# Optimization experiments

Hardware: AMD Instinct MI355X
Metric: run time of the kernel (lower is better)

The kernel has to match this reference:

```python
import jax, jax.numpy as jnp
import numpy as np

D, N = 512, 256          # transition steps, batch
H, L, V = 128, 64, 32000 # h_dim, label_dim, lexicon_size


def _valid_transitions(seed=0):
    # generate a valid shift/reduce schedule: reduce only when stack depth >= 2
    rng = np.random.default_rng(seed)
    ptr = np.zeros(N, np.int64)
    trans = np.zeros((D, N), np.int32)
    for t in range(D):
        r = ((rng.random(N) < 0.6) & (ptr >= 2)).astype(np.int32)
        trans[t] = r
        ptr += 1 - 2 * r  # every step pushes 1; reduce pops 2 first
    return jnp.asarray(trans)


def setup_inputs() -> dict:
    key = jax.random.key(0)
    k1, k2, k3 = jax.random.split(key, 3)
    transitions = _valid_transitions()
    labels_idx = jax.random.randint(k1, (D, N), 0, V, dtype=jnp.int32)
    emb = jax.random.normal(k2, (V, L), jnp.float32) * 0.02
    emb = emb.at[0].set(0.0)  # padding_idx=0
    arg_dim = L + 2 * H
    W = jax.random.normal(k3, (arg_dim, 5 * H), jnp.float32) / np.sqrt(arg_dim).astype(np.float32)
    b = jnp.zeros((5 * H,), jnp.float32)
    leaf = jnp.zeros((H,), jnp.float32)  # leaf_input placeholder vector
    return {"transitions": transitions, "labels_idx": labels_idx,
            "emb": emb, "W": W, "b": b, "leaf": leaf}


def _cell(x, hl, hr, cl, cr, W, b):
    # binary TreeLSTM (Tai et al.): gates from concat(label, h_left, h_right)
    g = jnp.concatenate([x, hl, hr], axis=-1) @ W + b  # [N, 5H]
    i, fl, fr, o, u = jnp.split(g, 5, axis=-1)
    c = jax.nn.sigmoid(i) * jnp.tanh(u) + jax.nn.sigmoid(fl) * cl + jax.nn.sigmoid(fr) * cr
    h = jax.nn.sigmoid(o) * jnp.tanh(c)
    return c, h


def reference(transitions, labels_idx, emb, W, b, leaf):
    labels = emb[labels_idx]  # [D,N,L]
    bidx = jnp.arange(N)

    def step(carry, inp):
        h_st, c_st, idx_st, ptr = carry  # [D,N,H],[D,N,H],[D,N],[N]
        t, mask, lab = inp
        mf = mask.astype(bool)[:, None]
        # right popped first, then left (matches _get_indices call order)
        ridx = idx_st[(ptr - 1) % D, bidx]
        lidx = idx_st[(ptr - 2) % D, bidx]
        hl = jnp.where(mf, h_st[lidx, bidx], leaf)
        hr = jnp.where(mf, h_st[ridx, bidx], leaf)
        cl = jnp.where(mf, c_st[lidx, bidx], leaf)
        cr = jnp.where(mf, c_st[ridx, bidx], leaf)
        c, h = _cell(lab, hl, hr, cl, cr, W, b)
        h_st = h_st.at[t].set(h)   # embeddings_stack[step] = h
        c_st = c_st.at[t].set(c)   # cells_stack[step] = c
        newptr = ptr - 2 * mask    # pops (if reduce)
        idx_st = idx_st.at[newptr, bidx].set(t)  # push current step for all batch
        return (h_st, c_st, idx_st, newptr + 1), None

    h_st = jnp.zeros((D, N, H), jnp.float32)
    c_st = jnp.zeros((D, N, H), jnp.float32)
    idx_st = jnp.zeros((D, N), jnp.int32)
    ptr = jnp.zeros((N,), jnp.int32)
    (h_st, c_st, _, _), _ = jax.lax.scan(
        step, (h_st, c_st, idx_st, ptr),
        (jnp.arange(D, dtype=jnp.int32), transitions, labels))
    # original returns (thin_stack[1][D-1], thin_stack[0][D-1]) = (cells, embeddings)
    return c_st[D - 1], h_st[D - 1]
```

## Files before the change

### kernel.cpp

```cpp
#include <hip/hip_runtime.h>
#include <stdint.h>


#define D     512
#define HD    128
#define LD    64
#define NTHR  512
#define GPR   328

typedef unsigned long long u64t;

__device__ __forceinline__ float sigf(float x){ return 1.0f/(1.0f+__expf(-x)); }
__device__ __forceinline__ float tanh_(float x){ return 1.0f-2.0f/(__expf(2.0f*x)+1.0f); }
__device__ __forceinline__ u64t gld64(const float* p){
  return __hip_atomic_load((const u64t*)p, __ATOMIC_RELAXED, __HIP_MEMORY_SCOPE_AGENT);
}
__device__ __forceinline__ u64t gld64u(const unsigned* p){
  return __hip_atomic_load((const u64t*)p, __ATOMIC_RELAXED, __HIP_MEMORY_SCOPE_AGENT);
}
__device__ __forceinline__ void gst32(float* p, float v){
  __hip_atomic_store(p, v, __ATOMIC_RELAXED, __HIP_MEMORY_SCOPE_AGENT);
}
__device__ __forceinline__ void gsttag(unsigned* p, unsigned v){
  __hip_atomic_store(p, v, __ATOMIC_RELAXED, __HIP_MEMORY_SCOPE_AGENT);
}

__global__ __launch_bounds__(NTHR,2) void spinn_kernel(
    const int* __restrict__ trans, const int* __restrict__ labels,
    const float* __restrict__ emb, const float* __restrict__ W,
    const float* __restrict__ bias, const float* __restrict__ leaf,
    float* __restrict__ out, unsigned* __restrict__ tags,
    float* __restrict__ rec, float* __restrict__ cown)
{
  const int bid = blockIdx.x;
  const int g2 = bid>>1, sl = bid&1, ps = sl^1;
  const int gb0 = g2*2;
  const int tid = threadIdx.x;
  const int kg = tid>>6, lane = tid&63;
  const int cq = lane;

  __shared__ __align__(16) float xs[2][2][320];
  __shared__ __align__(16) float gpq[16][GPR];
  __shared__ float bsl[320];
  __shared__ float lshd[HD];
  __shared__ float clb[2][2][64];
  __shared__ uint8_t mS[D][2];
  __shared__ short liA[D][2];
  __shared__ unsigned short stk_[2][D];

  float4 wr4[40]; float wr1[40];
  {
    const int gq = (cq>>4)*128 + sl*64 + ((cq*4)&63);
    const int gu = 512 + sl*64 + cq;
#pragma unroll
    for (int j=0;j<40;++j){
      int k = kg*40 + j;
      wr4[j] = *(const float4*)(W + (size_t)k*640 + gq);
      wr1[j] = W[(size_t)k*640 + gu];
    }
  }
  if (tid < 320){
    int c = tid;
    int gc = (c < 256) ? ((c>>6)*128 + sl*64 + (c&63)) : (512 + sl*64 + (c-256));
    bsl[c] = bias[gc];
  }
  if (tid < HD) lshd[tid] = leaf[tid];
  if (tid < 2){
    int b = tid, p = 0;
    for (int t=0;t<D;++t){
      int m = trans[t*256 + gb0 + b];
      short li = 0;
      if (m) li = (short)stk_[b][p-2];
      mS[t][b] = (uint8_t)m; liA[t][b] = li;
      int np = p - 2*m; stk_[b][np] = (unsigned short)t; p = np+1;
    }
  }
  __syncthreads();

  for (int idx = tid; idx < 640; idx += NTHR){
    int b = (idx >= 320) ? 1 : 0;
    int r = idx - b*320;
    if (r < 64){
      int row = labels[gb0 + b];
      xs[0][b][r] = emb[(size_t)row*LD + r];
    } else {
      xs[0][b][r] = lshd[(r-64)&127];
    }
  }
  __syncthreads();

  auto gemm = [&](int cur){
    float4 a0 = {0.f,0.f,0.f,0.f}, a1 = {0.f,0.f,0.f,0.f};
    float u0 = 0.f, u1 = 0.f;
#pragma unroll
    for (int j4=0;j4<10;++j4){
      int k = kg*40 + j4*4;
      float4 x0 = *(const float4*)&xs[cur][0][k];
      float4 x1 = *(const float4*)&xs[cur][1][k];
      float xa0[4] = {x0.x,x0.y,x0.z,x0.w};
      float xa1[4] = {x1.x,x1.y,x1.z,x1.w};
#pragma unroll
      for (int jj=0;jj<4;++jj){
        float4 w = wr4[j4*4+jj];
        float wu = wr1[j4*4+jj];
        a0.x = __builtin_fmaf(w.x, xa0[jj], a0.x);
        a0.y = __builtin_fmaf(w.y, xa0[jj], a0.y);
        a0.z = __builtin_fmaf(w.z, xa0[jj], a0.z);
        a0.w = __builtin_fmaf(w.w, xa0[jj], a0.w);
        a1.x = __builtin_fmaf(w.x, xa1[jj], a1.x);
        a1.y = __builtin_fmaf(w.y, xa1[jj], a1.y);
        a1.z = __builtin_fmaf(w.z, xa1[jj], a1.z);
        a1.w = __builtin_fmaf(w.w, xa1[jj], a1.w);
        u0 = __builtin_fmaf(wu, xa0[jj], u0);
        u1 = __builtin_fmaf(wu, xa1[jj], u1);
      }
    }
    *(float4*)&gpq[kg*2+0][cq*4] = a0;
    *(float4*)&gpq[kg*2+1][cq*4] = a1;
    gpq[kg*2+0][256+cq] = u0;
    gpq[kg*2+1][256+cq] = u1;
  };

  float ccprev = 0.f;

  for (int t=0;t<D;++t){
    const int cur = t&1, nxt = cur^1;

    if (kg < 4){
      gemm(cur);
    } else if (kg == 4){
      if (t+1 < D){
        int b = lane>>5, jj = lane&31;
        int row = labels[(t+1)*256 + gb0 + b];
        float2 ev = *(const float2*)(emb + (size_t)row*LD + jj*2);
        xs[nxt][b][jj*2]   = ev.x;
        xs[nxt][b][jj*2+1] = ev.y;
      }
    } else if (kg == 5){
      if (t+1 < D){
        int b = lane>>5, jj = lane&31;
        int m1 = mS[t+1][b]; int li = liA[t+1][b];
        if (m1){
          if (li <= t-2){
            size_t ro = (((size_t)li*128+g2)*2 + sl)*128 + b*64 + jj*2;
            union{u64t u; float f[2];} h_, c_;
            h_.u = gld64(rec + ro);
            c_.u = gld64(cown + ro);
            xs[nxt][b][64+sl*64+jj*2]   = h_.f[0];
            xs[nxt][b][64+sl*64+jj*2+1] = h_.f[1];
            clb[nxt][b][jj*2]   = c_.f[0];
            clb[nxt][b][jj*2+1] = c_.f[1];
          }
        } else {
          xs[nxt][b][64+sl*64+jj*2]   = lshd[sl*64+jj*2];
          xs[nxt][b][64+sl*64+jj*2+1] = lshd[sl*64+jj*2+1];
          clb[nxt][b][jj*2]   = lshd[sl*64+jj*2];
          clb[nxt][b][jj*2+1] = lshd[sl*64+jj*2+1];
        }
      }
    } else if (kg == 6){
      if (t+1 < D){
        int b = lane>>5, jj = lane&31;
        int m1 = mS[t+1][b]; int li = liA[t+1][b];
        if (m1){
          if (li <= t-2){
            size_t ro = (((size_t)li*128+g2)*2 + ps)*128 + b*64 + jj*2;
            union{u64t u; float f[2];} h_;
            h_.u = gld64(rec + ro);
            xs[nxt][b][64+ps*64+jj*2]   = h_.f[0];
            xs[nxt][b][64+ps*64+jj*2+1] = h_.f[1];
          }
        } else {
          xs[nxt][b][64+ps*64+jj*2]    = lshd[ps*64+jj*2];
          xs[nxt][b][64+ps*64+jj*2+1]  = lshd[ps*64+jj*2+1];
          xs[nxt][b][192+ps*64+jj*2]   = lshd[ps*64+jj*2];
          xs[nxt][b][192+ps*64+jj*2+1] = lshd[ps*64+jj*2+1];
        }
      }
    } else {
      if (t > 0){
        const unsigned* tp = tags + (((size_t)(t-1)*128+g2)*2 + ps)*16;
        u64t want = ((u64t)(unsigned)(t-1) << 32) | (unsigned)(t-1);
        int it = 0;
        while (gld64u(tp) != want){
          __builtin_amdgcn_s_sleep(1);
          if (++it > (1<<20)) break;
        }
        int b = lane>>5, jj = lane&31;
        size_t ro = (((size_t)(t-1)*128+g2)*2 + ps)*128 + lane*2;
        union{u64t u; float f[2];} h_;
        h_.u = gld64(rec + ro);
        if (mS[t][b]){
          xs[cur][b][192+ps*64+jj*2]   = h_.f[0];
          xs[cur][b][192+ps*64+jj*2+1] = h_.f[1];
        }
        if (t+1 < D && mS[t+1][b] && liA[t+1][b] == t-1){
          xs[nxt][b][64+ps*64+jj*2]   = h_.f[0];
          xs[nxt][b][64+ps*64+jj*2+1] = h_.f[1];
        }
      }
    }
    __syncthreads();

    if (kg >= 4){ gemm(cur); }
    __syncthreads();

    if (tid < 128){
      const int b = tid>>6, dl = tid&63, gd = sl*64+dl;
      const int m = mS[t][b];
      float s[5];
#pragma unroll
      for (int g=0; g<5; ++g){
        int c = (g<4) ? (g*64+dl) : (256+dl);
        float a = 0.f;
#pragma unroll
        for (int kk=0; kk<8; ++kk) a += gpq[kk*2+b][c];
        s[g] = a + bsl[c];
      }
      float cl_ = m ? clb[cur][b][dl] : lshd[gd];
      float cr_ = m ? ccprev : lshd[gd];
      float cc = sigf(s[0])*tanh_(s[4]) + sigf(s[1])*cl_ + sigf(s[2])*cr_;
      float hh = sigf(s[3])*tanh_(cc);
      ccprev = cc;
      size_t ro = (((size_t)t*128 + g2)*2 + sl)*128 + b*64 + dl;
      gst32(rec + ro, hh);
      gst32(cown + ro, cc);
      if (t == D-1){
        out[(size_t)(gb0+b)*HD + gd] = cc;
        out[(size_t)256*HD + (size_t)(gb0+b)*HD + gd] = hh;
      } else {
        xs[nxt][b][192+gd] = mS[t+1][b] ? hh : lshd[gd];
      }
      if (t+2 < D && mS[t+2][b] && liA[t+2][b] == t){
        xs[cur][b][64+gd]  = hh;
        clb[cur][b][dl]    = cc;
      }
      __asm__ volatile("s_waitcnt vmcnt(0)" ::: "memory");
      if (dl == 0)
        gsttag(tags + (((size_t)t*128+g2)*2+sl)*16 + b, (unsigned)t);
    }
    __syncthreads();
  }
}

extern "C" void kernel_launch(void* const* d_in, const int* in_sizes, int n_in,
                              void* d_out, int out_size, void* d_ws, size_t ws_size,
                              hipStream_t stream) {
  (void)in_sizes; (void)n_in; (void)out_size; (void)ws_size;
  const int*   trans  = (const int*)d_in[0];
  const int*   labels = (const int*)d_in[1];
  const float* emb    = (const float*)d_in[2];
  const float* W      = (const float*)d_in[3];
  const float* bias   = (const float*)d_in[4];
  const float* leaf   = (const float*)d_in[5];
  float* out = (float*)d_out;

  uint8_t* ws = (uint8_t*)d_ws;
  unsigned* tags = (unsigned*)ws;
  float* rec  = (float*)(ws + ((size_t)8<<20));
  float* cown = (float*)(ws + ((size_t)72<<20));

  spinn_kernel<<<dim3(256), dim3(NTHR), 0, stream>>>(
      trans, labels, emb, W, bias, leaf, out, tags, rec, cown);
}
```

Before: 1.997 ms.

## Replace flag-based cross-block handoff with tagged value ring and restructure step phases

```diff
diff --git a/kernel.cpp b/kernel.cpp
--- a/kernel.cpp
+++ b/kernel.cpp
@@ -15,21 +15,27 @@
 __device__ __forceinline__ u64t gld64(const float* p){
   return __hip_atomic_load((const u64t*)p, __ATOMIC_RELAXED, __HIP_MEMORY_SCOPE_AGENT);
 }
-__device__ __forceinline__ u64t gld64u(const unsigned* p){
-  return __hip_atomic_load((const u64t*)p, __ATOMIC_RELAXED, __HIP_MEMORY_SCOPE_AGENT);
+__device__ __forceinline__ u64t gld64r(const u64t* p){
+  return __hip_atomic_load(p, __ATOMIC_RELAXED, __HIP_MEMORY_SCOPE_AGENT);
 }
 __device__ __forceinline__ void gst32(float* p, float v){
   __hip_atomic_store(p, v, __ATOMIC_RELAXED, __HIP_MEMORY_SCOPE_AGENT);
 }
-__device__ __forceinline__ void gsttag(unsigned* p, unsigned v){
+__device__ __forceinline__ void gst64r(u64t* p, u64t v){
   __hip_atomic_store(p, v, __ATOMIC_RELAXED, __HIP_MEMORY_SCOPE_AGENT);
+}
+__device__ __forceinline__ u64t packw(float v, unsigned tg){
+  return ((u64t)tg << 32) | (u64t)__float_as_uint(v);
+}
+__device__ __forceinline__ float loww(u64t w){
+  return __uint_as_float((unsigned)(w & 0xffffffffu));
 }
 
 __global__ __launch_bounds__(NTHR,2) void spinn_kernel(
     const int* __restrict__ trans, const int* __restrict__ labels,
     const float* __restrict__ emb, const float* __restrict__ W,
     const float* __restrict__ bias, const float* __restrict__ leaf,
-    float* __restrict__ out, unsigned* __restrict__ tags,
+    float* __restrict__ out, u64t* __restrict__ ring,
     float* __restrict__ rec, float* __restrict__ cown)
 {
   const int bid = blockIdx.x;
@@ -126,9 +132,42 @@
   for (int t=0;t<D;++t){
     const int cur = t&1, nxt = cur^1;
 
-    if (kg < 4){
-      gemm(cur);
-    } else if (kg == 4){
+    gemm(cur);
+    __syncthreads();
+
+    if (tid < 128){
+      const int b = tid>>6, dl = tid&63, gd = sl*64+dl;
+      const int m = mS[t][b];
+      float s[5];
+#pragma unroll
+      for (int g=0; g<5; ++g){
+        int c = (g<4) ? (g*64+dl) : (256+dl);
+        float a = 0.f;
+#pragma unroll
+        for (int kk=0; kk<8; ++kk) a += gpq[kk*2+b][c];
+        s[g] = a + bsl[c];
+      }
+      float cl_ = m ? clb[cur][b][dl] : lshd[gd];
+      float cr_ = m ? ccprev : lshd[gd];
+      float cc = sigf(s[0])*tanh_(s[4]) + sigf(s[1])*cl_ + sigf(s[2])*cr_;
+      float hh = sigf(s[3])*tanh_(cc);
+      ccprev = cc;
+      gst64r(ring + (((size_t)(t&7)*128 + g2)*2 + sl)*128 + tid,
+             packw(hh, (unsigned)(t+1)));
+      size_t ro = (((size_t)t*128 + g2)*2 + sl)*128 + b*64 + dl;
+      gst32(rec + ro, hh);
+      gst32(cown + ro, cc);
+      if (t == D-1){
+        out[(size_t)(gb0+b)*HD + gd] = cc;
+        out[(size_t)256*HD + (size_t)(gb0+b)*HD + gd] = hh;
+      } else {
+        xs[nxt][b][192+gd] = mS[t+1][b] ? hh : lshd[gd];
+      }
+      if (t+2 < D && mS[t+2][b] && liA[t+2][b] == t){
+        xs[cur][b][64+gd]  = hh;
+        clb[cur][b][dl]    = cc;
+      }
+    } else if (kg == 2){
       if (t+1 < D){
         int b = lane>>5, jj = lane&31;
         int row = labels[(t+1)*256 + gb0 + b];
@@ -136,7 +175,7 @@
         xs[nxt][b][jj*2]   = ev.x;
         xs[nxt][b][jj*2+1] = ev.y;
       }
-    } else if (kg == 5){
+    } else if (kg == 3){
       if (t+1 < D){
         int b = lane>>5, jj = lane&31;
         int m1 = mS[t+1][b]; int li = liA[t+1][b];
@@ -169,75 +208,38 @@
             h_.u = gld64(rec + ro);
             xs[nxt][b][64+ps*64+jj*2]   = h_.f[0];
             xs[nxt][b][64+ps*64+jj*2+1] = h_.f[1];
+          } else {
+            const u64t* rp = ring + (((size_t)((t-1)&7)*128 + g2)*2 + ps)*128
+                             + b*64 + jj*2;
+            xs[nxt][b][64+ps*64+jj*2]   = loww(gld64r(rp));
+            xs[nxt][b][64+ps*64+jj*2+1] = loww(gld64r(rp+1));
           }
         } else {
-          xs[nxt][b][64+ps*64+jj*2]    = lshd[ps*64+jj*2];
-          xs[nxt][b][64+ps*64+jj*2+1]  = lshd[ps*64+jj*2+1];
+          xs[nxt][b][64+ps*64+jj*2]   = lshd[ps*64+jj*2];
+          xs[nxt][b][64+ps*64+jj*2+1] = lshd[ps*64+jj*2+1];
+        }
+      }
+    } else if (kg == 7){
+      if (t+1 < D){
+        const u64t* rp = ring + (((size_t)(t&7)*128 + g2)*2 + ps)*128 + lane*2;
+        const unsigned want = (unsigned)(t+1);
+        u64t w0 = 0, w1 = 0; int it = 0;
+        for (;;){
+          w0 = gld64r(rp); w1 = gld64r(rp+1);
+          int ok = ((unsigned)(w0>>32) == want) & ((unsigned)(w1>>32) == want);
+          if (__all(ok)) break;
+          __builtin_amdgcn_s_sleep(1);
+          if (++it > (1<<20)) break;
+        }
+        int b = lane>>5, jj = lane&31;
+        if (mS[t+1][b]){
+          xs[nxt][b][192+ps*64+jj*2]   = loww(w0);
+          xs[nxt][b][192+ps*64+jj*2+1] = loww(w1);
+        } else {
           xs[nxt][b][192+ps*64+jj*2]   = lshd[ps*64+jj*2];
           xs[nxt][b][192+ps*64+jj*2+1] = lshd[ps*64+jj*2+1];
         }
       }
-    } else {
-      if (t > 0){
-        const unsigned* tp = tags + (((size_t)(t-1)*128+g2)*2 + ps)*16;
-        u64t want = ((u64t)(unsigned)(t-1) << 32) | (unsigned)(t-1);
-        int it = 0;
-        while (gld64u(tp) != want){
-          __builtin_amdgcn_s_sleep(1);
-          if (++it > (1<<20)) break;
-        }
-        int b = lane>>5, jj = lane&31;
-        size_t ro = (((size_t)(t-1)*128+g2)*2 + ps)*128 + lane*2;
-        union{u64t u; float f[2];} h_;
-        h_.u = gld64(rec + ro);
-        if (mS[t][b]){
-          xs[cur][b][192+ps*64+jj*2]   = h_.f[0];
-          xs[cur][b][192+ps*64+jj*2+1] = h_.f[1];
-        }
-        if (t+1 < D && mS[t+1][b] && liA[t+1][b] == t-1){
-          xs[nxt][b][64+ps*64+jj*2]   = h_.f[0];
-          xs[nxt][b][64+ps*64+jj*2+1] = h_.f[1];
-        }
-      }
-    }
-    __syncthreads();
-
-    if (kg >= 4){ gemm(cur); }
-    __syncthreads();
-
-    if (tid < 128){
-      const int b = tid>>6, dl = tid&63, gd = sl*64+dl;
-      const int m = mS[t][b];
-      float s[5];
-#pragma unroll
-      for (int g=0; g<5; ++g){
-        int c = (g<4) ? (g*64+dl) : (256+dl);
-        float a = 0.f;
-#pragma unroll
-        for (int kk=0; kk<8; ++kk) a += gpq[kk*2+b][c];
-        s[g] = a + bsl[c];
-      }
-      float cl_ = m ? clb[cur][b][dl] : lshd[gd];
-      float cr_ = m ? ccprev : lshd[gd];
-      float cc = sigf(s[0])*tanh_(s[4]) + sigf(s[1])*cl_ + sigf(s[2])*cr_;
-      float hh = sigf(s[3])*tanh_(cc);
-      ccprev = cc;
-      size_t ro = (((size_t)t*128 + g2)*2 + sl)*128 + b*64 + dl;
-      gst32(rec + ro, hh);
-      gst32(cown + ro, cc);
-      if (t == D-1){
-        out[(size_t)(gb0+b)*HD + gd] = cc;
-        out[(size_t)256*HD + (size_t)(gb0+b)*HD + gd] = hh;
-      } else {
-        xs[nxt][b][192+gd] = mS[t+1][b] ? hh : lshd[gd];
-      }
-      if (t+2 < D && mS[t+2][b] && liA[t+2][b] == t){
-        xs[cur][b][64+gd]  = hh;
-        clb[cur][b][dl]    = cc;
-      }
-      __asm__ volatile("s_waitcnt vmcnt(0)" ::: "memory");
-      if (dl == 0)
-        gsttag(tags + (((size_t)t*128+g2)*2+sl)*16 + b, (unsigned)t);
     }
     __syncthreads();
   }
@@ -256,10 +258,10 @@
   float* out = (float*)d_out;
 
   uint8_t* ws = (uint8_t*)d_ws;
-  unsigned* tags = (unsigned*)ws;
+  u64t*  ring = (u64t*)ws;
   float* rec  = (float*)(ws + ((size_t)8<<20));
   float* cown = (float*)(ws + ((size_t)72<<20));
 
   spinn_kernel<<<dim3(256), dim3(NTHR), 0, stream>>>(
-      trans, labels, emb, W, bias, leaf, out, tags, rec, cown);
-}
+      trans, labels, emb, W, bias, leaf, out, ring, rec, cown);
+}
```

New measurement: 1.934 ms. -3.1%, faster.
